# Kernel optimization log

Measured on AMD Instinct MI355X. Metric: run time of the kernel, lower is better.

## Reference

```python
import jax, jax.numpy as jnp
import numpy as np

NUM_CLASSES = 512  # label_id values are in [0, NUM_CLASSES)
MARGIN = 1.0
EPS = 1e-6  # torch F.pairwise_distance default eps, added to the difference


def setup_inputs() -> dict:
    key = jax.random.key(0)
    k1, k2 = jax.random.split(key)
    N, D = 65536, 512
    output = jax.random.normal(k1, (N, D), dtype=jnp.float32)
    label_id = jax.random.randint(k2, (N,), 0, NUM_CLASSES, dtype=jnp.int64)
    return {"output": output, "label_id": label_id}


def reference(output, label_id):
    # Note: in the original torch code pre_class is never updated, so the
    # branch fires for EVERY sample i: per-sample class mean and
    # complement-class mean are gathered, giving [N, D] matrices.
    n = output.shape[0]
    # Per-class sums and counts in one segment-reduce pass.
    cls_sums = jax.ops.segment_sum(output, label_id, num_segments=NUM_CLASSES)      # [C, D]
    cls_cnts = jax.ops.segment_sum(jnp.ones((n,), output.dtype), label_id,
                                   num_segments=NUM_CLASSES)                        # [C]
    total = jnp.sum(output, axis=0)                                                 # [D]
    # Gather per-sample class stats (every present class has count >= 1).
    s = cls_sums[label_id]                 # [N, D] sum of own class
    c = cls_cnts[label_id][:, None]        # [N, 1] count of own class
    mu_pos = s / c                         # mean of samples with same label
    mu_neg = (total - s) / (n - c)         # mean of samples with different label
    # F.pairwise_distance(x, y) = || x - y + eps ||_2
    d = jnp.sqrt(jnp.sum((mu_pos - mu_neg + EPS) ** 2, axis=-1, keepdims=True))  # [N, 1]
    return jnp.mean(jnp.maximum(MARGIN - d, 0.0) ** 2)
```

## Files before the change

kernel.cpp:

```cpp
#include <hip/hip_runtime.h>

#define NCLS 512
#define DIM 512
#define NTHREADS 256
#define LIST_CAP 2048
#define EPS 1e-6f
#define MARGIN 1.0f

__global__ __launch_bounds__(NTHREADS)
void k_class_sums(const float* __restrict__ x, const int* __restrict__ lab,
                  float* __restrict__ cls_sums, int* __restrict__ cls_cnts, int N)
{
    const int c   = blockIdx.x;
    const int tid = threadIdx.x;

    __shared__ int s_list[LIST_CAP];
    __shared__ int s_cnt;
    if (tid == 0) s_cnt = 0;
    __syncthreads();

    float2 acc = make_float2(0.f, 0.f);
    int my_total = 0;

    const int4* lab4 = (const int4*)lab;
    const int nv = N >> 2;
    const float2* x2 = (const float2*)x;

    for (int base = 0; base < nv; base += NTHREADS) {
        const int j = base + tid;
        if (j < nv) {
            int4 l = lab4[j];
            int i0 = j << 2;
            if (l.x == c) s_list[atomicAdd(&s_cnt, 1)] = i0;
            if (l.y == c) s_list[atomicAdd(&s_cnt, 1)] = i0 + 1;
            if (l.z == c) s_list[atomicAdd(&s_cnt, 1)] = i0 + 2;
            if (l.w == c) s_list[atomicAdd(&s_cnt, 1)] = i0 + 3;
        }
        __syncthreads();
        const int cnt = s_cnt;
        __syncthreads();
        if (cnt > LIST_CAP - 4 * NTHREADS) {
            int r = 0;
            for (; r + 4 <= cnt; r += 4) {
                int r0 = s_list[r], r1 = s_list[r + 1], r2 = s_list[r + 2], r3 = s_list[r + 3];
                float2 v0 = x2[(size_t)r0 * (DIM / 2) + tid];
                float2 v1 = x2[(size_t)r1 * (DIM / 2) + tid];
                float2 v2 = x2[(size_t)r2 * (DIM / 2) + tid];
                float2 v3 = x2[(size_t)r3 * (DIM / 2) + tid];
                acc.x += v0.x + v1.x + v2.x + v3.x;
                acc.y += v0.y + v1.y + v2.y + v3.y;
            }
            for (; r < cnt; ++r) {
                float2 v = x2[(size_t)s_list[r] * (DIM / 2) + tid];
                acc.x += v.x; acc.y += v.y;
            }
            my_total += cnt;
            __syncthreads();
            if (tid == 0) s_cnt = 0;
            __syncthreads();
        }
    }

    {
        const int cnt = s_cnt;
        int r = 0;
        for (; r + 4 <= cnt; r += 4) {
            int r0 = s_list[r], r1 = s_list[r + 1], r2 = s_list[r + 2], r3 = s_list[r + 3];
            float2 v0 = x2[(size_t)r0 * (DIM / 2) + tid];
            float2 v1 = x2[(size_t)r1 * (DIM / 2) + tid];
            float2 v2 = x2[(size_t)r2 * (DIM / 2) + tid];
            float2 v3 = x2[(size_t)r3 * (DIM / 2) + tid];
            acc.x += v0.x + v1.x + v2.x + v3.x;
            acc.y += v0.y + v1.y + v2.y + v3.y;
        }
        for (; r < cnt; ++r) {
            float2 v = x2[(size_t)s_list[r] * (DIM / 2) + tid];
            acc.x += v.x; acc.y += v.y;
        }
        my_total += cnt;
    }

    ((float2*)cls_sums)[c * (DIM / 2) + tid] = acc;
    if (tid == 0) cls_cnts[c] = my_total;
}

__global__ __launch_bounds__(DIM)
void k_total(const float* __restrict__ cls_sums, float* __restrict__ total,
             float* __restrict__ d_out)
{
    const int d = threadIdx.x;
    float s0 = 0.f, s1 = 0.f, s2 = 0.f, s3 = 0.f;
    for (int c = 0; c < NCLS; c += 4) {
        s0 += cls_sums[(size_t)(c + 0) * DIM + d];
        s1 += cls_sums[(size_t)(c + 1) * DIM + d];
        s2 += cls_sums[(size_t)(c + 2) * DIM + d];
        s3 += cls_sums[(size_t)(c + 3) * DIM + d];
    }
    total[d] = (s0 + s1) + (s2 + s3);
    if (d == 0) d_out[0] = 0.f;
}

__global__ __launch_bounds__(NTHREADS)
void k_finalize(const float* __restrict__ cls_sums, const int* __restrict__ cls_cnts,
                const float* __restrict__ total, float* __restrict__ d_out, int N)
{
    const int c   = blockIdx.x;
    const int tid = threadIdx.x;
    const int cnt = cls_cnts[c];

    float2 s = ((const float2*)cls_sums)[c * (DIM / 2) + tid];
    float2 t = ((const float2*)total)[tid];

    float ss = 0.f;
    if (cnt > 0) {
        float inv_c  = 1.f / (float)cnt;
        float inv_nc = 1.f / (float)(N - cnt);
        float d0 = s.x * inv_c - (t.x - s.x) * inv_nc + EPS;
        float d1 = s.y * inv_c - (t.y - s.y) * inv_nc + EPS;
        ss = d0 * d0 + d1 * d1;
    }

    #pragma unroll
    for (int o = 1; o < 64; o <<= 1) ss += __shfl_xor(ss, o, 64);

    __shared__ float s_red[NTHREADS / 64];
    if ((tid & 63) == 0) s_red[tid >> 6] = ss;
    __syncthreads();

    if (tid == 0) {
        float tot = (s_red[0] + s_red[1]) + (s_red[2] + s_red[3]);
        float d = sqrtf(tot);
        float w = fmaxf(MARGIN - d, 0.f);
        float contrib = (float)cnt * w * w / (float)N;
        if (cnt > 0) atomicAdd(d_out, contrib);
    }
}

extern "C" void kernel_launch(void* const* d_in, const int* in_sizes, int n_in,
                              void* d_out, int out_size, void* d_ws, size_t ws_size,
                              hipStream_t stream)
{
    const float* x   = (const float*)d_in[0];
    const int*   lab = (const int*)d_in[1];
    float*       out = (float*)d_out;

    const int N = in_sizes[1];

    float* cls_sums = (float*)d_ws;
    float* total    = cls_sums + (size_t)NCLS * DIM;
    int*   cls_cnts = (int*)(total + DIM);

    k_class_sums<<<NCLS, NTHREADS, 0, stream>>>(x, lab, cls_sums, cls_cnts, N);
    k_total<<<1, DIM, 0, stream>>>(cls_sums, total, out);
    k_finalize<<<NCLS, NTHREADS, 0, stream>>>(cls_sums, cls_cnts, total, out, N);
}
```

Measured before the change: 79.23 us.

## Replace per-class label scans with histogram, prefix-sum, scatter, and sliced gather

Previously every class block scanned the full label array to build its own row list, so the labels were read 512 times. Now one block builds a label histogram and prefix sum, a scatter kernel writes row indices grouped by class, and the gather kernel sums each class's rows split over 4 column slices. The separate total-reduction kernel is dropped and totals are accumulated with float atomics. In exchange this adds a single-block histogram kernel, a contended atomic scatter, and summation order that depends on atomic ordering, so results are not bitwise deterministic.

```diff
diff --git a/kernel.cpp b/kernel.cpp
--- a/kernel.cpp
+++ b/kernel.cpp
@@ -2,137 +2,147 @@
 
 #define NCLS 512
 #define DIM 512
-#define NTHREADS 256
-#define LIST_CAP 2048
+#define D4 (DIM / 4)
+#define NSL 4
+#define SL_D4 (D4 / NSL)
 #define EPS 1e-6f
 #define MARGIN 1.0f
 
-__global__ __launch_bounds__(NTHREADS)
-void k_class_sums(const float* __restrict__ x, const int* __restrict__ lab,
-                  float* __restrict__ cls_sums, int* __restrict__ cls_cnts, int N)
+__global__ __launch_bounds__(1024)
+void k_prep(const int* __restrict__ lab, int N,
+            int* __restrict__ cnts, int* __restrict__ offsets, int* __restrict__ cur,
+            float* __restrict__ total, float* __restrict__ d_out)
 {
-    const int c   = blockIdx.x;
-    const int tid = threadIdx.x;
-
-    __shared__ int s_list[LIST_CAP];
-    __shared__ int s_cnt;
-    if (tid == 0) s_cnt = 0;
+    __shared__ int h[NCLS];
+    const int t = threadIdx.x;
+    if (t < NCLS) h[t] = 0;
     __syncthreads();
-
-    float2 acc = make_float2(0.f, 0.f);
-    int my_total = 0;
 
     const int4* lab4 = (const int4*)lab;
     const int nv = N >> 2;
-    const float2* x2 = (const float2*)x;
+    for (int j = t; j < nv; j += 1024) {
+        int4 l = lab4[j];
+        atomicAdd(&h[l.x], 1);
+        atomicAdd(&h[l.y], 1);
+        atomicAdd(&h[l.z], 1);
+        atomicAdd(&h[l.w], 1);
+    }
+    __syncthreads();
 
-    for (int base = 0; base < nv; base += NTHREADS) {
-        const int j = base + tid;
-        if (j < nv) {
-            int4 l = lab4[j];
-            int i0 = j << 2;
-            if (l.x == c) s_list[atomicAdd(&s_cnt, 1)] = i0;
-            if (l.y == c) s_list[atomicAdd(&s_cnt, 1)] = i0 + 1;
-            if (l.z == c) s_list[atomicAdd(&s_cnt, 1)] = i0 + 2;
-            if (l.w == c) s_list[atomicAdd(&s_cnt, 1)] = i0 + 3;
-        }
+    const int myc = (t < NCLS) ? h[t] : 0;
+
+    for (int o = 1; o < NCLS; o <<= 1) {
+        int add = 0;
+        if (t < NCLS && t >= o) add = h[t - o];
         __syncthreads();
-        const int cnt = s_cnt;
+        if (t < NCLS) h[t] += add;
         __syncthreads();
-        if (cnt > LIST_CAP - 4 * NTHREADS) {
-            int r = 0;
-            for (; r + 4 <= cnt; r += 4) {
-                int r0 = s_list[r], r1 = s_list[r + 1], r2 = s_list[r + 2], r3 = s_list[r + 3];
-                float2 v0 = x2[(size_t)r0 * (DIM / 2) + tid];
-                float2 v1 = x2[(size_t)r1 * (DIM / 2) + tid];
-                float2 v2 = x2[(size_t)r2 * (DIM / 2) + tid];
-                float2 v3 = x2[(size_t)r3 * (DIM / 2) + tid];
-                acc.x += v0.x + v1.x + v2.x + v3.x;
-                acc.y += v0.y + v1.y + v2.y + v3.y;
-            }
-            for (; r < cnt; ++r) {
-                float2 v = x2[(size_t)s_list[r] * (DIM / 2) + tid];
-                acc.x += v.x; acc.y += v.y;
-            }
-            my_total += cnt;
-            __syncthreads();
-            if (tid == 0) s_cnt = 0;
-            __syncthreads();
+    }
+
+    if (t < NCLS) {
+        const int excl = h[t] - myc;
+        cnts[t]    = myc;
+        offsets[t] = excl;
+        cur[t]     = excl;
+        total[t]   = 0.f;
+    }
+    if (t == 0) d_out[0] = 0.f;
+}
+
+__global__ __launch_bounds__(256)
+void k_scatter(const int* __restrict__ lab, int* __restrict__ cur,
+               int* __restrict__ sorted, int N)
+{
+    int i = blockIdx.x * blockDim.x + threadIdx.x;
+    const int stride = gridDim.x * blockDim.x;
+    for (; i < N; i += stride) {
+        const int c = lab[i];
+        const int p = atomicAdd(&cur[c], 1);
+        sorted[p] = i;
+    }
+}
+
+__global__ __launch_bounds__(256)
+void k_gather(const float4* __restrict__ x4, const int* __restrict__ sorted,
+              const int* __restrict__ offsets, const int* __restrict__ cnts,
+              float4* __restrict__ cls_sums4, float* __restrict__ total)
+{
+    const int b    = blockIdx.x;
+    const int c    = b >> 2;
+    const int sl   = b & 3;
+    const int t    = threadIdx.x;
+    const int d4   = t & (SL_D4 - 1);
+    const int rsub = t >> 5;
+    const int off  = offsets[c];
+    const int cnt  = cnts[c];
+    const int col  = sl * SL_D4 + d4;
+
+    float4 acc = make_float4(0.f, 0.f, 0.f, 0.f);
+    int r = rsub;
+    if (r < cnt) {
+        int row = sorted[off + r];
+        for (;;) {
+            const int nr = r + 8;
+            const int nrow = (nr < cnt) ? sorted[off + nr] : 0;
+            const float4 v = x4[(size_t)row * D4 + col];
+            acc.x += v.x; acc.y += v.y; acc.z += v.z; acc.w += v.w;
+            if (nr >= cnt) break;
+            r = nr; row = nrow;
         }
     }
 
-    {
-        const int cnt = s_cnt;
-        int r = 0;
-        for (; r + 4 <= cnt; r += 4) {
-            int r0 = s_list[r], r1 = s_list[r + 1], r2 = s_list[r + 2], r3 = s_list[r + 3];
-            float2 v0 = x2[(size_t)r0 * (DIM / 2) + tid];
-            float2 v1 = x2[(size_t)r1 * (DIM / 2) + tid];
-            float2 v2 = x2[(size_t)r2 * (DIM / 2) + tid];
-            float2 v3 = x2[(size_t)r3 * (DIM / 2) + tid];
-            acc.x += v0.x + v1.x + v2.x + v3.x;
-            acc.y += v0.y + v1.y + v2.y + v3.y;
+    __shared__ float4 red[256];
+    red[t] = acc;
+    __syncthreads();
+
+    if (t < SL_D4) {
+        float4 s = red[t];
+        #pragma unroll
+        for (int k = 1; k < 8; ++k) {
+            const float4 o = red[t + SL_D4 * k];
+            s.x += o.x; s.y += o.y; s.z += o.z; s.w += o.w;
         }
-        for (; r < cnt; ++r) {
-            float2 v = x2[(size_t)s_list[r] * (DIM / 2) + tid];
-            acc.x += v.x; acc.y += v.y;
-        }
-        my_total += cnt;
+        cls_sums4[(size_t)c * D4 + col] = s;
+        float* tp = total + col * 4;
+        atomicAdd(tp + 0, s.x);
+        atomicAdd(tp + 1, s.y);
+        atomicAdd(tp + 2, s.z);
+        atomicAdd(tp + 3, s.w);
     }
-
-    ((float2*)cls_sums)[c * (DIM / 2) + tid] = acc;
-    if (tid == 0) cls_cnts[c] = my_total;
 }
 
-__global__ __launch_bounds__(DIM)
-void k_total(const float* __restrict__ cls_sums, float* __restrict__ total,
-             float* __restrict__ d_out)
-{
-    const int d = threadIdx.x;
-    float s0 = 0.f, s1 = 0.f, s2 = 0.f, s3 = 0.f;
-    for (int c = 0; c < NCLS; c += 4) {
-        s0 += cls_sums[(size_t)(c + 0) * DIM + d];
-        s1 += cls_sums[(size_t)(c + 1) * DIM + d];
-        s2 += cls_sums[(size_t)(c + 2) * DIM + d];
-        s3 += cls_sums[(size_t)(c + 3) * DIM + d];
-    }
-    total[d] = (s0 + s1) + (s2 + s3);
-    if (d == 0) d_out[0] = 0.f;
-}
-
-__global__ __launch_bounds__(NTHREADS)
-void k_finalize(const float* __restrict__ cls_sums, const int* __restrict__ cls_cnts,
+__global__ __launch_bounds__(256)
+void k_finalize(const float* __restrict__ cls_sums, const int* __restrict__ cnts,
                 const float* __restrict__ total, float* __restrict__ d_out, int N)
 {
     const int c   = blockIdx.x;
     const int tid = threadIdx.x;
-    const int cnt = cls_cnts[c];
+    const int cnt = cnts[c];
 
-    float2 s = ((const float2*)cls_sums)[c * (DIM / 2) + tid];
-    float2 t = ((const float2*)total)[tid];
+    const float2 s = ((const float2*)cls_sums)[c * (DIM / 2) + tid];
+    const float2 t = ((const float2*)total)[tid];
 
     float ss = 0.f;
     if (cnt > 0) {
-        float inv_c  = 1.f / (float)cnt;
-        float inv_nc = 1.f / (float)(N - cnt);
-        float d0 = s.x * inv_c - (t.x - s.x) * inv_nc + EPS;
-        float d1 = s.y * inv_c - (t.y - s.y) * inv_nc + EPS;
+        const float inv_c  = 1.f / (float)cnt;
+        const float inv_nc = 1.f / (float)(N - cnt);
+        const float d0 = s.x * inv_c - (t.x - s.x) * inv_nc + EPS;
+        const float d1 = s.y * inv_c - (t.y - s.y) * inv_nc + EPS;
         ss = d0 * d0 + d1 * d1;
     }
 
     #pragma unroll
     for (int o = 1; o < 64; o <<= 1) ss += __shfl_xor(ss, o, 64);
 
-    __shared__ float s_red[NTHREADS / 64];
+    __shared__ float s_red[4];
     if ((tid & 63) == 0) s_red[tid >> 6] = ss;
     __syncthreads();
 
     if (tid == 0) {
-        float tot = (s_red[0] + s_red[1]) + (s_red[2] + s_red[3]);
-        float d = sqrtf(tot);
-        float w = fmaxf(MARGIN - d, 0.f);
-        float contrib = (float)cnt * w * w / (float)N;
-        if (cnt > 0) atomicAdd(d_out, contrib);
+        const float tot = (s_red[0] + s_red[1]) + (s_red[2] + s_red[3]);
+        const float d = sqrtf(tot);
+        const float w = fmaxf(MARGIN - d, 0.f);
+        if (cnt > 0) atomicAdd(d_out, (float)cnt * w * w / (float)N);
     }
 }
 
@@ -148,9 +158,14 @@
 
     float* cls_sums = (float*)d_ws;
     float* total    = cls_sums + (size_t)NCLS * DIM;
-    int*   cls_cnts = (int*)(total + DIM);
+    int*   cnts     = (int*)(total + DIM);
+    int*   offsets  = cnts + NCLS;
+    int*   cur      = offsets + NCLS;
+    int*   sorted   = cur + NCLS;
 
-    k_class_sums<<<NCLS, NTHREADS, 0, stream>>>(x, lab, cls_sums, cls_cnts, N);
-    k_total<<<1, DIM, 0, stream>>>(cls_sums, total, out);
-    k_finalize<<<NCLS, NTHREADS, 0, stream>>>(cls_sums, cls_cnts, total, out, N);
+    k_prep<<<1, 1024, 0, stream>>>(lab, N, cnts, offsets, cur, total, out);
+    k_scatter<<<64, 256, 0, stream>>>(lab, cur, sorted, N);
+    k_gather<<<NCLS * NSL, 256, 0, stream>>>((const float4*)x, sorted, offsets, cnts,
+                                             (float4*)cls_sums, total);
+    k_finalize<<<NCLS, 256, 0, stream>>>(cls_sums, cnts, total, out, N);
 }
```

New measurement: 108.8 us. 1.37x slower.
